# Kernel tuning notes

Hardware: AMD Instinct MI355X
Metric: run time of the kernel (lower is better)

The kernel has to match this reference:

```python
import jax, jax.numpy as jnp
import numpy as np

BLOCK_SIZE = 256


def setup_inputs() -> dict:
    key = jax.random.key(0)
    k1, k2, k3, k4 = jax.random.split(key, 4)
    B, T, C, H = 512, 256, 384, 64
    x = jax.random.normal(k1, (B, T, C), dtype=jnp.float32)
    Wk = jax.random.normal(k2, (H, C), dtype=jnp.float32) * (1.0 / np.sqrt(C))
    Wq = jax.random.normal(k3, (H, C), dtype=jnp.float32) * (1.0 / np.sqrt(C))
    Wv = jax.random.normal(k4, (H, C), dtype=jnp.float32) * (1.0 / np.sqrt(C))
    return {"x": x, "Wk": Wk, "Wq": Wq, "Wv": Wv}


def reference(x, Wk, Wq, Wv):
    # x: [B, T, C]; Wk/Wq/Wv: [H, C] (torch nn.Linear weight layout, bias=False)
    B, T, C = x.shape
    H = Wk.shape[0]
    k = jnp.einsum('btc,hc->bth', x, Wk)
    q = jnp.einsum('btc,hc->bth', x, Wq)
    v = jnp.einsum('btc,hc->bth', x, Wv)
    scale = 1.0 / jnp.sqrt(jnp.float32(H))
    scores = jnp.einsum('bqh,bkh->bqk', q, k) * scale  # [B, T, T]
    causal = jnp.tril(jnp.ones((T, T), dtype=bool))
    scores = jnp.where(causal, scores, -jnp.inf)
    weights = jax.nn.softmax(scores, axis=-1)
    # dropout is identity in eval mode
    out = jnp.einsum('bqk,bkh->bqh', weights, v)  # [B, T, H]
    return out
```

## Files before the change

kernel.cpp:

```cpp
#include <hip/hip_runtime.h>
#include <hip/hip_bf16.h>
#include <math.h>

#define TT 256
#define CC 384
#define HH 64

typedef float v4f   __attribute__((ext_vector_type(4)));
typedef short short8 __attribute__((ext_vector_type(8)));

#define MFMA(a, b, c) __builtin_amdgcn_mfma_f32_16x16x32_bf16((a), (b), (c), 0, 0, 0)

__device__ __forceinline__ unsigned short f2bf(float f) {
    unsigned int u = __float_as_uint(f);
    u += 0x7FFFu + ((u >> 16) & 1u);
    return (unsigned short)(u >> 16);
}

__device__ __forceinline__ ushort4 f2bf4(float4 f) {
    union { __hip_bfloat162 h2[2]; ushort4 u4; } cv;
    cv.h2[0] = __float22bfloat162_rn(make_float2(f.x, f.y));
    cv.h2[1] = __float22bfloat162_rn(make_float2(f.z, f.w));
    return cv.u4;
}

#define QSCALE 0.18033688f

__global__ __launch_bounds__(512, 4)
void qkv_proj(const float* __restrict__ x, const float* __restrict__ Wkp,
              const float* __restrict__ Wqp, const float* __restrict__ Wvp,
              unsigned short* __restrict__ qg, unsigned short* __restrict__ kg,
              unsigned short* __restrict__ vtg)
{
    __shared__ unsigned short sm[17408];
    unsigned short* x_s = sm;
    unsigned short* w_s = sm + 5120;
    unsigned short* epi = sm;

    const int tid  = threadIdx.x;
    const int wave = tid >> 6;
    const int lane = tid & 63;
    const int col  = lane & 15;
    const int quad = lane >> 4;
    const int row0 = blockIdx.x * 128;

    const int lr  = tid >> 3;
    const int lc4 = (tid & 7) * 4;

    const float* xp  = x   + (size_t)(row0 + lr) * CC + lc4;
    const float* wqp = Wqp + (size_t)lr * CC + lc4;
    const float* wkp = Wkp + (size_t)lr * CC + lc4;
    const float* wvp = Wvp + (size_t)lr * CC + lc4;

    v4f acc[12];
    #pragma unroll
    for (int j = 0; j < 12; ++j) acc[j] = (v4f){0.f, 0.f, 0.f, 0.f};

    float4 xA0 = *(const float4*)(xp);
    float4 xA1 = *(const float4*)(xp + 64 * CC);
    float4 wqA = *(const float4*)(wqp);
    float4 wkA = *(const float4*)(wkp);
    float4 wvA = *(const float4*)(wvp);

    const int afrag_off = (wave * 16 + col) * 40 + quad * 8;

    #pragma unroll
    for (int s = 0; s < 12; ++s) {
        float4 xB0, xB1, wqB, wkB, wvB;
        if (s < 11) {
            const int k0 = (s + 1) * 32;
            xB0 = *(const float4*)(xp + k0);
            xB1 = *(const float4*)(xp + 64 * CC + k0);
            wqB = *(const float4*)(wqp + k0);
            wkB = *(const float4*)(wkp + k0);
            wvB = *(const float4*)(wvp + k0);
        }
        __syncthreads();
        *(ushort4*)&x_s[lr * 40 + lc4]         = f2bf4(xA0);
        *(ushort4*)&x_s[(lr + 64) * 40 + lc4]  = f2bf4(xA1);
        *(ushort4*)&w_s[lr * 40 + lc4]         = f2bf4(wqA);
        *(ushort4*)&w_s[(64 + lr) * 40 + lc4]  = f2bf4(wkA);
        *(ushort4*)&w_s[(128 + lr) * 40 + lc4] = f2bf4(wvA);
        __syncthreads();
        const short8 a = *(const short8*)&x_s[afrag_off];
        #pragma unroll
        for (int nt = 0; nt < 12; ++nt) {
            const short8 bf = *(const short8*)&w_s[(nt * 16 + col) * 40 + quad * 8];
            acc[nt] = MFMA(a, bf, acc[nt]);
        }
        if (s < 11) { xA0 = xB0; xA1 = xB1; wqA = wqB; wkA = wkB; wvA = wvB; }
    }

    const int b    = row0 >> 8;
    const int half = (row0 >> 7) & 1;

    __syncthreads();
    #pragma unroll
    for (int nt = 0; nt < 8; ++nt) {
        #pragma unroll
        for (int r = 0; r < 4; ++r) {
            const int rl = wave * 16 + quad * 4 + r;
            const int n  = nt * 16 + col;
            float v = acc[nt][r];
            if (nt < 4) v *= QSCALE;
            epi[rl * 136 + n] = f2bf(v);
        }
    }
    __syncthreads();
    #pragma unroll
    for (int p = 0; p < 4; ++p) {
        const int idx = tid + p * 512;
        const int r = idx >> 4, ch = idx & 15;
        const short8 v = *(const short8*)&epi[r * 136 + ch * 8];
        const size_t base = (size_t)(row0 + r) * 64 + (ch & 7) * 8;
        if (ch < 8) *(short8*)&qg[base] = v;
        else        *(short8*)&kg[base] = v;
    }

    __syncthreads();
    #pragma unroll
    for (int nt = 8; nt < 12; ++nt) {
        #pragma unroll
        for (int r = 0; r < 4; ++r) {
            const int rl = wave * 16 + quad * 4 + r;
            const int h  = nt * 16 + col - 128;
            epi[h * 136 + rl] = f2bf(acc[nt][r]);
        }
    }
    __syncthreads();
    #pragma unroll
    for (int p = 0; p < 2; ++p) {
        const int idx = tid + p * 512;
        const int h = idx >> 4, ch = idx & 15;
        const short8 v = *(const short8*)&epi[h * 136 + ch * 8];
        *(short8*)&vtg[((size_t)b * 64 + h) * 256 + half * 128 + ch * 8] = v;
    }
}

__global__ __launch_bounds__(256, 4)
void attn(const unsigned short* __restrict__ qg, const unsigned short* __restrict__ kg,
          const unsigned short* __restrict__ vtg, float* __restrict__ out)
{
    __shared__ unsigned short Pb_all[4 * 16 * 40];
    const int tid  = threadIdx.x;
    const int wave = tid >> 6;
    const int lane = tid & 63;
    const int col  = lane & 15;
    const int quad = lane >> 4;
    const int id   = blockIdx.x;
    const int b    = (id & 7) * 64 + (id >> 4);
    const int g    = (id >> 3) & 1;

    unsigned short* Pb = Pb_all + wave * 640;
    const unsigned short* kb_base = kg  + (size_t)b * 256 * 64;
    const unsigned short* vt_base = vtg + (size_t)b * 64 * 256;

    #pragma unroll
    for (int mi = 0; mi < 2; ++mi) {
        const int j  = g * 4 + wave;
        const int qt = mi ? (15 - j) : j;
        const size_t qoff = ((size_t)b * 256 + qt * 16 + col) * 64 + quad * 8;
        const short8 aq0 = *(const short8*)(qg + qoff);
        const short8 aq1 = *(const short8*)(qg + qoff + 32);

        float lsum[4];
        v4f oacc[4];
        #pragma unroll
        for (int r = 0; r < 4; ++r) lsum[r] = 0.f;
        #pragma unroll
        for (int hn = 0; hn < 4; ++hn) oacc[hn] = (v4f){0.f, 0.f, 0.f, 0.f};

        const int nch = qt / 2 + 1;
        short8 b00, b01, b10, b11;
        {
            const int ko0 = col * 64 + quad * 8;
            const int ko1 = (16 + col) * 64 + quad * 8;
            b00 = *(const short8*)(kb_base + ko0);
            b01 = *(const short8*)(kb_base + ko0 + 32);
            b10 = *(const short8*)(kb_base + ko1);
            b11 = *(const short8*)(kb_base + ko1 + 32);
        }
        for (int kc = 0; kc < nch; ++kc) {
            const int kb = kc * 32;
            v4f s0 = (v4f){0.f, 0.f, 0.f, 0.f};
            v4f s1 = (v4f){0.f, 0.f, 0.f, 0.f};
            s0 = MFMA(aq0, b00, s0);
            s0 = MFMA(aq1, b01, s0);
            s1 = MFMA(aq0, b10, s1);
            s1 = MFMA(aq1, b11, s1);
            if (kc + 1 < nch) {
                const int ko0 = (kb + 32 + col) * 64 + quad * 8;
                const int ko1 = (kb + 48 + col) * 64 + quad * 8;
                b00 = *(const short8*)(kb_base + ko0);
                b01 = *(const short8*)(kb_base + ko0 + 32);
                b10 = *(const short8*)(kb_base + ko1);
                b11 = *(const short8*)(kb_base + ko1 + 32);
            }
            const bool diag = (kc == qt / 2);
            #pragma unroll
            for (int r = 0; r < 4; ++r) {
                const int t = qt * 16 + quad * 4 + r;
                float v0 = s0[r];
                float v1 = s1[r];
                if (diag) {
                    if (kb + col > t)      v0 = -1e30f;
                    if (kb + 16 + col > t) v1 = -1e30f;
                }
                const float p0 = exp2f(v0);
                const float p1 = exp2f(v1);
                lsum[r] += p0 + p1;
                Pb[(quad * 4 + r) * 40 + col]      = f2bf(p0);
                Pb[(quad * 4 + r) * 40 + 16 + col] = f2bf(p1);
            }
            __threadfence_block();
            const short8 ap = *(const short8*)&Pb[col * 40 + quad * 8];
            #pragma unroll
            for (int hn = 0; hn < 4; ++hn) {
                const short8 bv = *(const short8*)(vt_base + (hn * 16 + col) * 256 + kb + quad * 8);
                oacc[hn] = MFMA(ap, bv, oacc[hn]);
            }
        }

        #pragma unroll
        for (int r = 0; r < 4; ++r) {
            float l = lsum[r];
            l += __shfl_xor(l, 1);
            l += __shfl_xor(l, 2);
            l += __shfl_xor(l, 4);
            l += __shfl_xor(l, 8);
            const int t = qt * 16 + quad * 4 + r;
            const float inv = 1.0f / l;
            float* op = out + ((size_t)b * TT + t) * HH;
            #pragma unroll
            for (int hn = 0; hn < 4; ++hn)
                op[hn * 16 + col] = oacc[hn][r] * inv;
        }
    }
}

extern "C" void kernel_launch(void* const* d_in, const int* in_sizes, int n_in,
                              void* d_out, int out_size, void* d_ws, size_t ws_size,
                              hipStream_t stream) {
    const float* x  = (const float*)d_in[0];
    const float* Wk = (const float*)d_in[1];
    const float* Wq = (const float*)d_in[2];
    const float* Wv = (const float*)d_in[3];
    float* out = (float*)d_out;

    unsigned short* qg  = (unsigned short*)d_ws;
    unsigned short* kg  = qg + (size_t)512 * 256 * 64;
    unsigned short* vtg = kg + (size_t)512 * 256 * 64;

    qkv_proj<<<dim3(1024), dim3(512), 0, stream>>>(x, Wk, Wq, Wv, qg, kg, vtg);
    attn<<<dim3(1024), dim3(256), 0, stream>>>(qg, kg, vtg, out);
}
```

Baseline: 337.0 us.

## Compute transposed scores so P feeds PV MFMA from registers, dropping LDS

Swaps the MFMA operand order so each lane holds scores for one query row over four consecutive keys. That lets the exponentiated probabilities be packed straight into bf16 A-operands for 16x16x16 MFMAs with no LDS round trip and no fence. V loads become 4-element loads issued ahead of the score MFMAs, and the row-sum reduction changes to cross-quad shuffles plus a broadcast. The cost is twice as many, narrower PV MFMAs and smaller global loads.

```diff
diff --git a/kernel.cpp b/kernel.cpp
--- a/kernel.cpp
+++ b/kernel.cpp
@@ -8,8 +8,10 @@
 
 typedef float v4f   __attribute__((ext_vector_type(4)));
 typedef short short8 __attribute__((ext_vector_type(8)));
-
-#define MFMA(a, b, c) __builtin_amdgcn_mfma_f32_16x16x32_bf16((a), (b), (c), 0, 0, 0)
+typedef short bh4   __attribute__((ext_vector_type(4)));
+
+#define MFMA(a, b, c)   __builtin_amdgcn_mfma_f32_16x16x32_bf16((a), (b), (c), 0, 0, 0)
+#define MFMA16(a, b, c) __builtin_amdgcn_mfma_f32_16x16x16bf16_1k((a), (b), (c), 0, 0, 0)
 
 __device__ __forceinline__ unsigned short f2bf(float f) {
     unsigned int u = __float_as_uint(f);
@@ -22,6 +24,13 @@
     cv.h2[0] = __float22bfloat162_rn(make_float2(f.x, f.y));
     cv.h2[1] = __float22bfloat162_rn(make_float2(f.z, f.w));
     return cv.u4;
+}
+
+__device__ __forceinline__ bh4 pack4(float a, float b, float c, float d) {
+    union { __hip_bfloat162 h2[2]; bh4 s; } cv;
+    cv.h2[0] = __float22bfloat162_rn(make_float2(a, b));
+    cv.h2[1] = __float22bfloat162_rn(make_float2(c, d));
+    return cv.s;
 }
 
 #define QSCALE 0.18033688f
@@ -141,17 +150,16 @@
 void attn(const unsigned short* __restrict__ qg, const unsigned short* __restrict__ kg,
           const unsigned short* __restrict__ vtg, float* __restrict__ out)
 {
-    __shared__ unsigned short Pb_all[4 * 16 * 40];
     const int tid  = threadIdx.x;
     const int wave = tid >> 6;
     const int lane = tid & 63;
     const int col  = lane & 15;
     const int quad = lane >> 4;
+    const int q4   = quad * 4;
     const int id   = blockIdx.x;
     const int b    = (id & 7) * 64 + (id >> 4);
     const int g    = (id >> 3) & 1;
 
-    unsigned short* Pb = Pb_all + wave * 640;
     const unsigned short* kb_base = kg  + (size_t)b * 256 * 64;
     const unsigned short* vt_base = vtg + (size_t)b * 64 * 256;
 
@@ -159,14 +167,13 @@
     for (int mi = 0; mi < 2; ++mi) {
         const int j  = g * 4 + wave;
         const int qt = mi ? (15 - j) : j;
+        const int qrow = qt * 16 + col;
         const size_t qoff = ((size_t)b * 256 + qt * 16 + col) * 64 + quad * 8;
         const short8 aq0 = *(const short8*)(qg + qoff);
         const short8 aq1 = *(const short8*)(qg + qoff + 32);
 
-        float lsum[4];
+        float lsum = 0.f;
         v4f oacc[4];
-        #pragma unroll
-        for (int r = 0; r < 4; ++r) lsum[r] = 0.f;
         #pragma unroll
         for (int hn = 0; hn < 4; ++hn) oacc[hn] = (v4f){0.f, 0.f, 0.f, 0.f};
 
@@ -182,12 +189,19 @@
         }
         for (int kc = 0; kc < nch; ++kc) {
             const int kb = kc * 32;
-            v4f s0 = (v4f){0.f, 0.f, 0.f, 0.f};
-            v4f s1 = (v4f){0.f, 0.f, 0.f, 0.f};
-            s0 = MFMA(aq0, b00, s0);
-            s0 = MFMA(aq1, b01, s0);
-            s1 = MFMA(aq0, b10, s1);
-            s1 = MFMA(aq1, b11, s1);
+            bh4 bv0[4], bv1[4];
+            #pragma unroll
+            for (int hn = 0; hn < 4; ++hn) {
+                const unsigned short* vp = vt_base + (hn * 16 + col) * 256 + kb + q4;
+                bv0[hn] = *(const bh4*)(vp);
+                bv1[hn] = *(const bh4*)(vp + 16);
+            }
+            v4f st0 = (v4f){0.f, 0.f, 0.f, 0.f};
+            v4f st1 = (v4f){0.f, 0.f, 0.f, 0.f};
+            st0 = MFMA(b00, aq0, st0);
+            st0 = MFMA(b01, aq1, st0);
+            st1 = MFMA(b10, aq0, st1);
+            st1 = MFMA(b11, aq1, st1);
             if (kc + 1 < nch) {
                 const int ko0 = (kb + 32 + col) * 64 + quad * 8;
                 const int ko1 = (kb + 48 + col) * 64 + quad * 8;
@@ -197,39 +211,35 @@
                 b11 = *(const short8*)(kb_base + ko1 + 32);
             }
             const bool diag = (kc == qt / 2);
+            float p0[4], p1[4];
             #pragma unroll
             for (int r = 0; r < 4; ++r) {
-                const int t = qt * 16 + quad * 4 + r;
-                float v0 = s0[r];
-                float v1 = s1[r];
+                float v0 = st0[r];
+                float v1 = st1[r];
                 if (diag) {
-                    if (kb + col > t)      v0 = -1e30f;
-                    if (kb + 16 + col > t) v1 = -1e30f;
+                    if (kb + q4 + r > qrow)      v0 = -1e30f;
+                    if (kb + 16 + q4 + r > qrow) v1 = -1e30f;
                 }
-                const float p0 = exp2f(v0);
-                const float p1 = exp2f(v1);
-                lsum[r] += p0 + p1;
-                Pb[(quad * 4 + r) * 40 + col]      = f2bf(p0);
-                Pb[(quad * 4 + r) * 40 + 16 + col] = f2bf(p1);
-            }
-            __threadfence_block();
-            const short8 ap = *(const short8*)&Pb[col * 40 + quad * 8];
+                p0[r] = exp2f(v0);
+                p1[r] = exp2f(v1);
+                lsum += p0[r] + p1[r];
+            }
+            const bh4 P0 = pack4(p0[0], p0[1], p0[2], p0[3]);
+            const bh4 P1 = pack4(p1[0], p1[1], p1[2], p1[3]);
             #pragma unroll
             for (int hn = 0; hn < 4; ++hn) {
-                const short8 bv = *(const short8*)(vt_base + (hn * 16 + col) * 256 + kb + quad * 8);
-                oacc[hn] = MFMA(ap, bv, oacc[hn]);
-            }
-        }
-
+                oacc[hn] = MFMA16(P0, bv0[hn], oacc[hn]);
+                oacc[hn] = MFMA16(P1, bv1[hn], oacc[hn]);
+            }
+        }
+
+        float l = lsum;
+        l += __shfl_xor(l, 16);
+        l += __shfl_xor(l, 32);
         #pragma unroll
         for (int r = 0; r < 4; ++r) {
-            float l = lsum[r];
-            l += __shfl_xor(l, 1);
-            l += __shfl_xor(l, 2);
-            l += __shfl_xor(l, 4);
-            l += __shfl_xor(l, 8);
-            const int t = qt * 16 + quad * 4 + r;
-            const float inv = 1.0f / l;
+            const float inv = 1.0f / __shfl(l, q4 + r);
+            const int t = qt * 16 + q4 + r;
             float* op = out + ((size_t)b * TT + t) * HH;
             #pragma unroll
             for (int hn = 0; hn < 4; ++hn)
```

New measurement: 349.7 us. 1.04x slower.
